# Kernel tuning notes

Hardware: AMD Instinct MI355X
Metric: run time of the kernel (lower is better)

The kernel has to match this reference:

```python
import jax, jax.numpy as jnp
import numpy as np

B, S, E, H = 16, 2048, 512, 64


def setup_inputs() -> dict:
    key = jax.random.key(0)
    k1, k2, k3, k4, k5 = jax.random.split(key, 5)
    inp = {
        "input": jax.random.normal(k1, (B, S, E), dtype=jnp.float32),
        "seq_lengths": jax.random.randint(k2, (B,), 0, S).astype(jnp.int64),
        "Wq": jax.random.normal(k3, (E, H), dtype=jnp.float32) * (1.0 / np.sqrt(E)),
        "Wk": jax.random.normal(k4, (E, H), dtype=jnp.float32) * (1.0 / np.sqrt(E)),
        "Wv": jax.random.normal(k5, (E, H), dtype=jnp.float32) * (1.0 / np.sqrt(E)),
    }
    return inp


def reference(input, seq_lengths, Wq, Wk, Wv):
    # Projections (bias-free Linear): [B,S,E] @ [E,H] -> [B,S,H]
    q = input @ Wq
    k = input @ Wk
    v = input @ Wv
    Sdim = input.shape[1]
    head_size = Wk.shape[-1]
    # Padding mask: position >= seq_length -> True. Zero out q and k (NOT v),
    # exactly as the torch module does with masked_fill.
    pad = (jnp.arange(Sdim)[None, :] >= seq_lengths[:, None])[:, :, None]  # [B,S,1]
    q = jnp.where(pad, 0.0, q)
    k = jnp.where(pad, 0.0, k)
    scale = 1.0 / np.sqrt(head_size).astype(np.float32)
    # Full score matrix [B,S,S] (the memory-bound intermediate)
    scores = jnp.einsum("bsh,bth->bst", q, k) * scale
    weights = jax.nn.softmax(scores, axis=-1)
    weights = jnp.where(jnp.isnan(weights), 0.0, weights)
    out = jnp.einsum("bst,bth->bsh", weights, v)  # [B,S,H]
    return out
```

## Files before the change

### kernel.cpp

```cpp
#include <hip/hip_runtime.h>
#include <hip/hip_bf16.h>

typedef __bf16 bf16;
typedef __bf16 bf16x8 __attribute__((ext_vector_type(8)));
typedef __bf16 bf16x4 __attribute__((ext_vector_type(4)));
typedef float  f32x4  __attribute__((ext_vector_type(4)));
typedef float  f32x16 __attribute__((ext_vector_type(16)));
typedef unsigned int u32x4 __attribute__((ext_vector_type(4)));

static constexpr int SDIM = 2048;
static constexpr int EDIM = 512;
static constexpr int HDIM = 64;

typedef __attribute__((address_space(1))) const void* gptr_t;
typedef __attribute__((address_space(3))) void*       lptr_t;

__device__ __forceinline__ void gl_lds16(const bf16* g, bf16* l) {
  __builtin_amdgcn_global_load_lds((gptr_t)g, (lptr_t)l, 16, 0, 0);
}

#if __has_builtin(__builtin_amdgcn_exp2f)
#define EXP2F(x) __builtin_amdgcn_exp2f(x)
#else
#define EXP2F(x) exp2f(x)
#endif

__device__ __forceinline__ bf16x8 pack8(f32x4 a, f32x4 b) {
  bf16x8 r;
  r[0] = (bf16)a[0]; r[1] = (bf16)a[1]; r[2] = (bf16)a[2]; r[3] = (bf16)a[3];
  r[4] = (bf16)b[0]; r[5] = (bf16)b[1]; r[6] = (bf16)b[2]; r[7] = (bf16)b[3];
  return r;
}

__device__ __forceinline__ unsigned cvtpk_bf16(float a, float b) {
  unsigned r;
  asm("v_cvt_pk_bf16_f32 %0, %1, %2" : "=v"(r) : "v"(a), "v"(b));
  return r;
}

__global__ __launch_bounds__(256) void wt_kernel(const float* __restrict__ Wq,
                                                 const float* __restrict__ Wk,
                                                 const float* __restrict__ Wv,
                                                 bf16* __restrict__ Wt) {
  __shared__ float lds[64][65];
  const int mat = blockIdx.x >> 3;
  const int et  = blockIdx.x & 7;
  const float* W = (mat == 0) ? Wq : ((mat == 1) ? Wk : Wv);
  const float scale = (mat == 0) ? 0.18033688f : 1.0f;
  const int t  = threadIdx.x;
  const int er = t >> 2;
  const int c4 = (t & 3) * 16;
#pragma unroll
  for (int j = 0; j < 4; ++j) {
    f32x4 v = *(const f32x4*)(W + (size_t)(et * 64 + er) * HDIM + c4 + j * 4);
    lds[er][c4 + j * 4 + 0] = v[0]; lds[er][c4 + j * 4 + 1] = v[1];
    lds[er][c4 + j * 4 + 2] = v[2]; lds[er][c4 + j * 4 + 3] = v[3];
  }
  __syncthreads();
  const int h  = t >> 2;
  const int ec = (t & 3) * 16;
  bf16x8 o0, o1;
#pragma unroll
  for (int j = 0; j < 8; ++j) o0[j] = (bf16)(lds[ec + j][h] * scale);
#pragma unroll
  for (int j = 0; j < 8; ++j) o1[j] = (bf16)(lds[ec + 8 + j][h] * scale);
  bf16* dst = Wt + mat * (HDIM * EDIM) + (size_t)h * EDIM + et * 64 + ec;
  *(bf16x8*)dst = o0;
  *(bf16x8*)(dst + 8) = o1;
}

__global__ __launch_bounds__(256) void proj_kernel(const float* __restrict__ x,
                                                   const bf16* __restrict__ Wt,
                                                   const int* __restrict__ lens,
                                                   bf16* __restrict__ qo,
                                                   bf16* __restrict__ ko,
                                                   bf16* __restrict__ vT) {
  __shared__ __align__(16) bf16 wbuf[2][192 * 64];
  const int tid  = threadIdx.x;
  const int wave = tid >> 6;
  const int lane = tid & 63;
  const int quad = lane >> 4;
  const int l16  = lane & 15;
  const int rowbase = blockIdx.x * 64 + wave * 16;
  const int b = blockIdx.x >> 5;
  const float* xrow = x + (size_t)(rowbase + l16) * EDIM + quad * 8;
  const int srow   = lane >> 3;
  const int schunk = (lane & 7) ^ srow;

  #define WSTAGE(ck, buf) { _Pragma("unroll")                                  \
    for (int i6 = 0; i6 < 6; ++i6) {                                           \
      const int R0 = (wave * 6 + i6) * 8;                                      \
      gl_lds16(Wt + (size_t)(R0 + srow) * EDIM + (ck) * 64 + schunk * 8,       \
               &(buf)[R0 * 64]); } }

  f32x4 acc[3][4];
#pragma unroll
  for (int m = 0; m < 3; ++m)
#pragma unroll
    for (int nt = 0; nt < 4; ++nt) acc[m][nt] = (f32x4){0.f, 0.f, 0.f, 0.f};

  #define WCOMPUTE(buf, eo4, afrag) { _Pragma("unroll")                        \
    for (int m = 0; m < 3; ++m) { _Pragma("unroll")                            \
      for (int nt = 0; nt < 4; ++nt) {                                         \
        bf16x8 bfv = *(const bf16x8*)(&(buf)[(m * 64 + nt * 16 + l16) * 64 +   \
                                             ((((eo4) + quad) ^ (l16 & 7)) * 8)]); \
        acc[m][nt] = __builtin_amdgcn_mfma_f32_16x16x32_bf16(afrag, bfv, acc[m][nt], 0, 0, 0); } } }

  WSTAGE(0, wbuf[0]);
  f32x4 xA0 = *(const f32x4*)(xrow);
  f32x4 xB0 = *(const f32x4*)(xrow + 4);
  f32x4 xA1 = *(const f32x4*)(xrow + 32);
  f32x4 xB1 = *(const f32x4*)(xrow + 36);
#pragma unroll 2
  for (int ck = 0; ck < 8; ++ck) {
    __syncthreads();
    const int ksn = (ck < 7) ? (ck + 1) * 2 : 14;
    f32x4 nA0 = *(const f32x4*)(xrow + ksn * 32);
    f32x4 nB0 = *(const f32x4*)(xrow + ksn * 32 + 4);
    f32x4 nA1 = *(const f32x4*)(xrow + ksn * 32 + 32);
    f32x4 nB1 = *(const f32x4*)(xrow + ksn * 32 + 36);
    if (ck + 1 < 8) WSTAGE(ck + 1, wbuf[(ck + 1) & 1]);
    bf16x8 a = pack8(xA0, xB0);
    WCOMPUTE(wbuf[ck & 1], 0, a);
    a = pack8(xA1, xB1);
    WCOMPUTE(wbuf[ck & 1], 4, a);
    xA0 = nA0; xB0 = nB0; xA1 = nA1; xB1 = nB1;
  }

  int odd_or = 0;
#pragma unroll
  for (int i = 1; i < 16; i += 2) odd_or |= lens[i];
  const int len = (odd_or == 0) ? lens[2 * b] : lens[b];

#pragma unroll
  for (int nt = 0; nt < 4; ++nt) {
    const int h = nt * 16 + l16;
    bf16x4 vv;
#pragma unroll
    for (int r = 0; r < 4; ++r) {
      const int row = rowbase + quad * 4 + r;
      const int s = row & (SDIM - 1);
      const bool pad = (s >= len);
      qo[(size_t)row * HDIM + h] = (bf16)(pad ? 0.f : acc[0][nt][r]);
      ko[(size_t)row * HDIM + h] = (bf16)(pad ? 0.f : acc[1][nt][r]);
      vv[r] = (bf16)acc[2][nt][r];
    }
    *(bf16x4*)(vT + ((size_t)b * HDIM + h) * SDIM + (rowbase & (SDIM - 1)) + quad * 4) = vv;
  }
  #undef WSTAGE
  #undef WCOMPUTE
}

__global__ __launch_bounds__(256) void attn_kernel(const bf16* __restrict__ qb,
                                                   const bf16* __restrict__ kb,
                                                   const bf16* __restrict__ vT,
                                                   float* __restrict__ out) {
  __shared__ __align__(16) bf16 Kbuf[2][2][64 * 64];
  __shared__ __align__(16) bf16 Vbuf[2][2][64 * 64];
  const int tid  = threadIdx.x;
  const int wave = tid >> 6;
  const int lane = tid & 63;
  const int hi   = lane >> 5;
  const int l32  = lane & 31;
  const int iq   = wave & 1;
  const int jk   = wave >> 1;
  const int xcd = blockIdx.x & 7;
  const int jj  = blockIdx.x >> 3;
  const int b   = xcd * 2 + (jj >> 5);
  const int qbase = (jj & 31) * 64 + iq * 32;
  const bf16* q0 = qb + (size_t)b * SDIM * HDIM;
  const bf16* k0 = kb + (size_t)b * SDIM * HDIM;
  const bf16* v0 = vT + (size_t)b * HDIM * SDIM;
  const int srow   = lane >> 3;
  const int schunk = (lane & 7) ^ srow;
  const int rswz   = (l32 & 7) << 4;

  bf16x8 qf[4];
#pragma unroll
  for (int c = 0; c < 4; ++c)
    qf[c] = *(const bf16x8*)(q0 + (size_t)(qbase + l32) * HDIM + c * 16 + hi * 8);

  f32x16 O[2];
#pragma unroll
  for (int ht = 0; ht < 2; ++ht)
#pragma unroll
    for (int r = 0; r < 16; ++r) O[ht][r] = 0.f;
  float l_acc = 0.f;

  #define STAGE(sidx, db) {                                                    \
    const int key0_ = (wave & 1) * 1024 + (sidx) * 64;                         \
    if (wave < 2) {                                                            \
      const bf16* gk = k0 + (size_t)(key0_ + srow) * HDIM + schunk * 8;        \
      bf16* lk = &Kbuf[db][wave & 1][0];                                       \
      _Pragma("unroll")                                                        \
      for (int r8 = 0; r8 < 8; ++r8)                                           \
        gl_lds16(gk + (size_t)r8 * 8 * HDIM, lk + r8 * 8 * 64);                \
    } else {                                                                   \
      const bf16* gv = v0 + (size_t)srow * SDIM + key0_ + schunk * 8;          \
      bf16* lv = &Vbuf[db][wave & 1][0];                                       \
      _Pragma("unroll")                                                        \
      for (int r8 = 0; r8 < 8; ++r8)                                           \
        gl_lds16(gv + (size_t)r8 * 8 * SDIM, lv + r8 * 8 * 64);                \
    }                                                                          \
  }

  STAGE(0, 0);
#pragma unroll 2
  for (int s = 0; s < 16; ++s) {
    __syncthreads();
    if (s + 1 < 16) STAGE(s + 1, (s + 1) & 1);
    const bf16* KB = &Kbuf[s & 1][jk][0];
    const bf16* VB = &Vbuf[s & 1][jk][0];

    bf16x8 pa[4];
#pragma unroll
    for (int kt = 0; kt < 2; ++kt) {
      f32x16 st;
#pragma unroll
      for (int r = 0; r < 16; ++r) st[r] = 0.f;
      const int krow = kt * 32 + l32;
#pragma unroll
      for (int c = 0; c < 4; ++c) {
        bf16x8 kf = *(const bf16x8*)((const char*)KB + krow * 128 +
                                     ((c * 32 + hi * 16) ^ rswz));
        st = __builtin_amdgcn_mfma_f32_32x32x16_bf16(kf, qf[c], st, 0, 0, 0);
      }
      float p[16];
#pragma unroll
      for (int r = 0; r < 16; ++r) p[r] = EXP2F(st[r]);
      float s0 = (p[0] + p[1]) + (p[2] + p[3]);
      float s1 = (p[4] + p[5]) + (p[6] + p[7]);
      float s2 = (p[8] + p[9]) + (p[10] + p[11]);
      float s3 = (p[12] + p[13]) + (p[14] + p[15]);
      l_acc += (s0 + s1) + (s2 + s3);
      unsigned u0 = cvtpk_bf16(p[0], p[1]);
      unsigned u1 = cvtpk_bf16(p[2], p[3]);
      unsigned u2 = cvtpk_bf16(p[4], p[5]);
      unsigned u3 = cvtpk_bf16(p[6], p[7]);
      asm("v_permlane32_swap_b32 %0, %1" : "+v"(u0), "+v"(u2));
      asm("v_permlane32_swap_b32 %0, %1" : "+v"(u1), "+v"(u3));
      union { u32x4 u; bf16x8 v; } f0;
      f0.u[0] = u0; f0.u[1] = u1; f0.u[2] = u2; f0.u[3] = u3;
      pa[kt * 2 + 0] = f0.v;
      unsigned u4 = cvtpk_bf16(p[8],  p[9]);
      unsigned u5 = cvtpk_bf16(p[10], p[11]);
      unsigned u6 = cvtpk_bf16(p[12], p[13]);
      unsigned u7 = cvtpk_bf16(p[14], p[15]);
      asm("v_permlane32_swap_b32 %0, %1" : "+v"(u4), "+v"(u6));
      asm("v_permlane32_swap_b32 %0, %1" : "+v"(u5), "+v"(u7));
      union { u32x4 u; bf16x8 v; } f1;
      f1.u[0] = u4; f1.u[1] = u5; f1.u[2] = u6; f1.u[3] = u7;
      pa[kt * 2 + 1] = f1.v;
    }
#pragma unroll
    for (int ht = 0; ht < 2; ++ht) {
      const int vrow = ht * 32 + l32;
#pragma unroll
      for (int tc = 0; tc < 4; ++tc) {
        bf16x8 vf = *(const bf16x8*)((const char*)VB + vrow * 128 +
                                     ((tc * 32 + hi * 16) ^ rswz));
        O[ht] = __builtin_amdgcn_mfma_f32_32x32x16_bf16(pa[tc], vf, O[ht], 0, 0, 0);
      }
    }
  }

  l_acc += __shfl_xor(l_acc, 32);

  float* cb = (float*)&Kbuf[0][0][0];
  float* cl = (float*)&Vbuf[0][0][0];
  __syncthreads();
  if (jk == 1) {
#pragma unroll
    for (int ht = 0; ht < 2; ++ht)
#pragma unroll
      for (int r = 0; r < 16; ++r) {
        const int qrow = (r & 3) + 8 * (r >> 2) + 4 * hi;
        cb[(iq * 32 + qrow) * 64 + ht * 32 + l32] = O[ht][r];
      }
    if (hi == 0) cl[iq * 32 + l32] = l_acc;
  }
  __syncthreads();
  if (jk == 0) {
    const float inv_own = 1.0f / (l_acc + cl[iq * 32 + l32]);
#pragma unroll
    for (int r = 0; r < 16; ++r) {
      const int qrow = (r & 3) + 8 * (r >> 2) + 4 * hi;
      const float inv = __shfl(inv_own, qrow);
#pragma unroll
      for (int ht = 0; ht < 2; ++ht) {
        const float val = (O[ht][r] + cb[(iq * 32 + qrow) * 64 + ht * 32 + l32]) * inv;
        out[((size_t)b * SDIM + qbase + qrow) * HDIM + ht * 32 + l32] = val;
      }
    }
  }
  #undef STAGE
}

extern "C" void kernel_launch(void* const* d_in, const int* in_sizes, int n_in,
                              void* d_out, int out_size, void* d_ws, size_t ws_size,
                              hipStream_t stream) {
  (void)in_sizes; (void)n_in; (void)out_size; (void)ws_size;
  const float* x  = (const float*)d_in[0];
  const int*   sl = (const int*)d_in[1];
  const float* Wq = (const float*)d_in[2];
  const float* Wk = (const float*)d_in[3];
  const float* Wv = (const float*)d_in[4];
  float* out = (float*)d_out;

  char* ws = (char*)d_ws;
  bf16* Wt = (bf16*)(ws);
  bf16* qb = (bf16*)(ws + (256 << 10));
  bf16* kb = (bf16*)(ws + (256 << 10) + (4 << 20));
  bf16* vT = (bf16*)(ws + (256 << 10) + (8 << 20));

  wt_kernel  <<<24,  256, 0, stream>>>(Wq, Wk, Wv, Wt);
  proj_kernel<<<512, 256, 0, stream>>>(x, Wt, sl, qb, kb, vT);
  attn_kernel<<<512, 256, 0, stream>>>(qb, kb, vT, out);
}
```

Baseline: 136.9 us.

## Deepen projection prefetch pipeline with explicit vmcnt waits and barriers

Restructures the QKV projection main loop so that x-row register loads are prefetched two chunks ahead instead of one. Each iteration now ends with an explicit s_waitcnt vmcnt plus raw s_barrier, replacing __syncthreads at the top of the loop, and sched_barriers pin the instruction order. The goal is to keep more global loads in flight and stop the compiler from inserting conservative full waits. The cost is extra live registers, and correctness now rests on hand-counted vmcnt values. The last iteration redundantly restages chunk 7 into the unused buffer.

```diff
diff --git a/kernel.cpp b/kernel.cpp
--- a/kernel.cpp
+++ b/kernel.cpp
@@ -107,24 +107,40 @@
         acc[m][nt] = __builtin_amdgcn_mfma_f32_16x16x32_bf16(afrag, bfv, acc[m][nt], 0, 0, 0); } } }
 
   WSTAGE(0, wbuf[0]);
-  f32x4 xA0 = *(const f32x4*)(xrow);
-  f32x4 xB0 = *(const f32x4*)(xrow + 4);
-  f32x4 xA1 = *(const f32x4*)(xrow + 32);
-  f32x4 xB1 = *(const f32x4*)(xrow + 36);
-#pragma unroll 2
+  __builtin_amdgcn_sched_barrier(0);
+  f32x4 c0 = *(const f32x4*)(xrow);
+  f32x4 c1 = *(const f32x4*)(xrow + 4);
+  f32x4 c2 = *(const f32x4*)(xrow + 32);
+  f32x4 c3 = *(const f32x4*)(xrow + 36);
+  f32x4 n0 = *(const f32x4*)(xrow + 64);
+  f32x4 n1 = *(const f32x4*)(xrow + 68);
+  f32x4 n2 = *(const f32x4*)(xrow + 96);
+  f32x4 n3 = *(const f32x4*)(xrow + 100);
+  __builtin_amdgcn_sched_barrier(0);
+  asm volatile("s_waitcnt vmcnt(8)" ::: "memory");
+  __builtin_amdgcn_s_barrier();
+  __builtin_amdgcn_sched_barrier(0);
+
+#pragma unroll
   for (int ck = 0; ck < 8; ++ck) {
-    __syncthreads();
-    const int ksn = (ck < 7) ? (ck + 1) * 2 : 14;
-    f32x4 nA0 = *(const f32x4*)(xrow + ksn * 32);
-    f32x4 nB0 = *(const f32x4*)(xrow + ksn * 32 + 4);
-    f32x4 nA1 = *(const f32x4*)(xrow + ksn * 32 + 32);
-    f32x4 nB1 = *(const f32x4*)(xrow + ksn * 32 + 36);
-    if (ck + 1 < 8) WSTAGE(ck + 1, wbuf[(ck + 1) & 1]);
-    bf16x8 a = pack8(xA0, xB0);
+    const int cs = (ck < 7) ? (ck + 1) : 7;
+    WSTAGE(cs, wbuf[(ck + 1) & 1]);
+    __builtin_amdgcn_sched_barrier(0);
+    const int kf = (ck < 6) ? (ck + 2) : 7;
+    f32x4 m0 = *(const f32x4*)(xrow + kf * 64);
+    f32x4 m1 = *(const f32x4*)(xrow + kf * 64 + 4);
+    f32x4 m2 = *(const f32x4*)(xrow + kf * 64 + 32);
+    f32x4 m3 = *(const f32x4*)(xrow + kf * 64 + 36);
+    __builtin_amdgcn_sched_barrier(0);
+    bf16x8 a = pack8(c0, c1);
     WCOMPUTE(wbuf[ck & 1], 0, a);
-    a = pack8(xA1, xB1);
+    a = pack8(c2, c3);
     WCOMPUTE(wbuf[ck & 1], 4, a);
-    xA0 = nA0; xB0 = nB0; xA1 = nA1; xB1 = nB1;
+    c0 = n0; c1 = n1; c2 = n2; c3 = n3;
+    n0 = m0; n1 = m1; n2 = m2; n3 = m3;
+    asm volatile("s_waitcnt vmcnt(4)" ::: "memory");
+    __builtin_amdgcn_s_barrier();
+    __builtin_amdgcn_sched_barrier(0);
   }
 
   int odd_or = 0;
```

Measured after the change: 135.9 us. No clear change (-0.8%).
